# Performance work log

Hardware: AMD Instinct MI355X
Metric: run time of the kernel (lower is better)

## Reference

```python
import jax, jax.numpy as jnp
import numpy as np

L, D, V, F4 = 12, 768, 50304, 3072
B, T = 4, 1024


def setup_inputs() -> dict:
    key = jax.random.key(0)
    ks = jax.random.split(key, 12)
    s = 0.02
    return {
        "idx": jax.random.randint(ks[0], (B, T), 0, V),
        "targets": jax.random.randint(ks[1], (B, T), 0, V),
        "wte": jax.random.normal(ks[2], (V, D), jnp.float32) * s,  # tied with lm_head
        "pos_embed": jax.random.normal(ks[3], (L, D), jnp.float32),  # per-block (1,1,D) learned pos embed
        "dyt_alpha": jnp.full((L, 3), 0.5, jnp.float32),  # dyt, dyt2, dyt3 alphas
        "dyt_w": jnp.ones((L, 3, D), jnp.float32),
        "dyt_b": jnp.zeros((L, 3, D), jnp.float32),
        "Wq": jax.random.normal(ks[4], (L, D, D), jnp.float32) * s,
        "Wk": jax.random.normal(ks[5], (L, D, D), jnp.float32) * s,
        "Wv": jax.random.normal(ks[6], (L, D, D), jnp.float32) * s,
        "Wp": jax.random.normal(ks[7], (L, D, D), jnp.float32) * s,
        "bp": jnp.zeros((L, D), jnp.float32),
        "We": jax.random.normal(ks[8], (L, F4, D), jnp.float32) * s,
        "be": jnp.zeros((L, F4), jnp.float32),
        "Wc": jax.random.normal(ks[9], (L, D, F4), jnp.float32) * s,
        "bc": jnp.zeros((L, D), jnp.float32),
    }


def _dyt(x, a, w, b):
    return jnp.tanh(a * x) * w + b


def _forward(idx, targets, wte, pos_embed, dyt_alpha, dyt_w, dyt_b,
             Wq, Wk, Wv, Wp, bp, We, be, Wc, bc):
    b, t = idx.shape
    x = wte[idx]  # (b,t,D)
    pos = jnp.arange(t)
    pbias = -jnp.abs(pos[None, :] - pos[:, None]).astype(x.dtype)  # (t,t) ALiBi-style bias
    scale = 1.0 / np.sqrt(D)  # note: source scales by sqrt(emb_dim), not head dim
    total_kl = jnp.asarray(0.0, x.dtype)
    for l in range(L):
        xl = x + pos_embed[l][None, None, :]
        prior = _dyt(xl, dyt_alpha[l, 2], dyt_w[l, 2], dyt_b[l, 2])  # dyt3
        h = _dyt(xl, dyt_alpha[l, 0], dyt_w[l, 0], dyt_b[l, 0])      # dyt (dropout=0)
        Q = jnp.einsum('btd,od->bto', h, Wq[l])
        K = jnp.einsum('btd,od->bto', h, Wk[l])
        Vv = jnp.einsum('btd,od->bto', h, Wv[l])
        scores = jnp.einsum('btd,bsd->bts', Q, K) * scale + pbias  # (b,t,t), no causal mask
        aw = jax.nn.softmax(scores, axis=-1)
        ao = jnp.einsum('bts,bsd->btd', aw, Vv)
        ao = jnp.einsum('btd,od->bto', ao, Wp[l]) + bp[l]
        h2 = _dyt(ao, dyt_alpha[l, 1], dyt_w[l, 1], dyt_b[l, 1])     # dyt2
        h2 = jax.nn.gelu(jnp.einsum('btd,fd->btf', h2, We[l]) + be[l], approximate=False)
        h2 = jnp.einsum('btf,df->btd', h2, Wc[l]) + bc[l]
        posterior = h2 + prior
        m = 0.5 * (prior + posterior)
        lm = jax.nn.log_softmax(m, axis=-1)
        mp = jnp.exp(lm)
        lp = jax.nn.log_softmax(prior, axis=-1)
        lq = jax.nn.log_softmax(posterior, axis=-1)
        # F.kl_div(log_p, q, reduction='batchmean') = sum(q*(log q - log_p)) / batch
        kl = 0.5 * (jnp.sum(mp * (lm - lp)) + jnp.sum(mp * (lm - lq))) / b
        total_kl = total_kl + kl
        x = posterior
    logits = jnp.einsum('btd,vd->btv', x[:, -1:, :], wte)  # (b,1,V)
    full_logits = jnp.einsum('btd,vd->btv', x, wte)
    lsm = jax.nn.log_softmax(full_logits, axis=-1)
    nll = -jnp.take_along_axis(lsm, targets[..., None], axis=-1).squeeze(-1)
    loss = jnp.mean(nll) + total_kl * 0.1
    return logits, loss


def reference(idx, targets, wte, pos_embed, dyt_alpha, dyt_w, dyt_b,
              Wq, Wk, Wv, Wp, bp, We, be, Wc, bc):
    return _forward(idx, targets, wte, pos_embed, dyt_alpha, dyt_w, dyt_b,
                    Wq, Wk, Wv, Wp, bp, We, be, Wc, bc)
```

## Files before the change

### kernel.cpp

```cpp
#include <hip/hip_runtime.h>
#include <hip/hip_bf16.h>

typedef __attribute__((ext_vector_type(8))) short bf16x8;
typedef __attribute__((ext_vector_type(4))) float f32x4;

__device__ __forceinline__ short f2bf(float f) {
  unsigned u = __float_as_uint(f);
  u = u + 0x7fffu + ((u >> 16) & 1u);
  return (short)(u >> 16);
}
__device__ __forceinline__ float bf2f(short s) {
  return __uint_as_float(((unsigned)(unsigned short)s) << 16);
}

#define GLOB_CAST(p) ((const __attribute__((address_space(1))) void*)(p))
#define LDS_CAST(p) ((__attribute__((address_space(3))) void*)(p))
#define GLL16(g, l) __builtin_amdgcn_global_load_lds(GLOB_CAST(g), LDS_CAST(l), 16, 0, 0)

constexpr int EP_BF16 = 0, EP_SCORES = 1, EP_DYT = 2, EP_GELU = 3, EP_PRIOR = 4;

__global__ __launch_bounds__(256) void cvt_k(const float* __restrict__ src,
                                             short* __restrict__ dst, long n4) {
  const long s = (long)blockIdx.x * 256 + threadIdx.x;
  if (s >= n4) return;
  float4 v = ((const float4*)src)[s];
  short4 o = {f2bf(v.x), f2bf(v.y), f2bf(v.z), f2bf(v.w)};
  ((short4*)dst)[s] = o;
}

__global__ __launch_bounds__(256) void cvt_layer_k(
    const float* __restrict__ wq, const float* __restrict__ wk,
    const float* __restrict__ wv, const float* __restrict__ wp,
    const float* __restrict__ we, const float* __restrict__ wc,
    short* __restrict__ dst) {
  const long s = (long)blockIdx.x * 256 + threadIdx.x;
  const long e = s * 4;
  const float* src; long off;
  if (e < 589824)        { src = wq; off = e; }
  else if (e < 1179648)  { src = wk; off = e - 589824; }
  else if (e < 1769472)  { src = wv; off = e - 1179648; }
  else if (e < 2359296)  { src = wp; off = e - 1769472; }
  else if (e < 4718592)  { src = we; off = e - 2359296; }
  else                   { src = wc; off = e - 4718592; }
  float4 v = *(const float4*)(src + off);
  short4 o = {f2bf(v.x), f2bf(v.y), f2bf(v.z), f2bf(v.w)};
  *(short4*)(dst + e) = o;
}

__global__ __launch_bounds__(256) void embed_head_k(
    const int* __restrict__ idx, const float* __restrict__ wte,
    const float* __restrict__ pos, const float* __restrict__ alp,
    const float* __restrict__ w, const float* __restrict__ b,
    float* __restrict__ x, float* __restrict__ prior, short* __restrict__ h) {
  const long s = (long)blockIdx.x * 256 + threadIdx.x;
  const long row = s / 192;
  const int c4 = (int)(s % 192);
  float4 xv = ((const float4*)(wte + (long)idx[row] * 768))[c4];
  ((float4*)x)[s] = xv;
  float4 pv = ((const float4*)pos)[c4];
  float4 w0 = ((const float4*)w)[c4];
  float4 b0 = ((const float4*)b)[c4];
  float4 w2 = ((const float4*)(w + 1536))[c4];
  float4 b2 = ((const float4*)(b + 1536))[c4];
  const float a0 = alp[0], a2 = alp[2];
  float4 xl = {xv.x + pv.x, xv.y + pv.y, xv.z + pv.z, xv.w + pv.w};
  float4 pr = {tanhf(a2 * xl.x) * w2.x + b2.x, tanhf(a2 * xl.y) * w2.y + b2.y,
               tanhf(a2 * xl.z) * w2.z + b2.z, tanhf(a2 * xl.w) * w2.w + b2.w};
  ((float4*)prior)[s] = pr;
  short4 hh = {f2bf(tanhf(a0 * xl.x) * w0.x + b0.x),
               f2bf(tanhf(a0 * xl.y) * w0.y + b0.y),
               f2bf(tanhf(a0 * xl.z) * w0.z + b0.z),
               f2bf(tanhf(a0 * xl.w) * w0.w + b0.w)};
  ((short4*)h)[s] = hh;
}

template <int EP, int TN>
__global__ __launch_bounds__(256, 2) void gemm_bt(
    const short* __restrict__ A, const short* __restrict__ B,
    void* __restrict__ Cv, int K, int lda, int ldb, int ldc,
    long sA, long sB, long sC,
    const float* __restrict__ bias, const float* __restrict__ dw,
    const float* __restrict__ db, const float* __restrict__ alp,
    const float* __restrict__ prior, float scale) {
  constexpr int NF = TN / 32;
  __shared__ short As[128 * 64];
  __shared__ short Bs[TN * 64];
  const int tid = threadIdx.x, lane = tid & 63;
  const int wr = tid >> 7, wc = (tid >> 6) & 1;
  const long rowBase = (long)blockIdx.y * 128;
  const long colBase = (long)blockIdx.x * TN;
  const short* Ab = A + (long)blockIdx.z * sA;
  const short* Bb = B + (long)blockIdx.z * sB;
  const int srow = tid >> 3, sseg = tid & 7;
  const int ssegS = sseg ^ (srow & 7);

  f32x4 acc[4][NF];
#pragma unroll
  for (int m = 0; m < 4; ++m)
#pragma unroll
    for (int n = 0; n < NF; ++n) acc[m][n] = (f32x4){0.f, 0.f, 0.f, 0.f};

  const int q = lane >> 4, cl = lane & 15;
  const int rsw = cl & 7;

  for (int kt = 0; kt < K; kt += 64) {
#pragma unroll
    for (int i = 0; i < 4; ++i)
      GLL16(Ab + (rowBase + i * 32 + srow) * (long)lda + kt + ssegS * 8,
            As + ((i * 32 + srow) * 64 + sseg * 8));
#pragma unroll
    for (int i = 0; i < TN / 32; ++i)
      GLL16(Bb + (colBase + i * 32 + srow) * (long)ldb + kt + ssegS * 8,
            Bs + ((i * 32 + srow) * 64 + sseg * 8));
    __syncthreads();
#pragma unroll
    for (int kk = 0; kk < 2; ++kk) {
      const int sw = ((kk * 4 + q) ^ rsw) << 3;
      bf16x8 af[4], bfr[NF];
#pragma unroll
      for (int m = 0; m < 4; ++m)
        af[m] = *(const bf16x8*)&As[(wr * 64 + m * 16 + cl) * 64 + sw];
#pragma unroll
      for (int n = 0; n < NF; ++n)
        bfr[n] = *(const bf16x8*)&Bs[(wc * (TN / 2) + n * 16 + cl) * 64 + sw];
#pragma unroll
      for (int m = 0; m < 4; ++m)
#pragma unroll
        for (int n = 0; n < NF; ++n)
          acc[m][n] = __builtin_amdgcn_mfma_f32_16x16x32_bf16(af[m], bfr[n], acc[m][n], 0, 0, 0);
    }
    __syncthreads();
  }

#pragma unroll
  for (int m = 0; m < 4; ++m) {
#pragma unroll
    for (int n = 0; n < NF; ++n) {
#pragma unroll
      for (int j = 0; j < 4; ++j) {
        long r = rowBase + wr * 64 + m * 16 + q * 4 + j;
        long c = colBase + wc * (TN / 2) + n * 16 + cl;
        float v = acc[m][n][j];
        if constexpr (EP == EP_SCORES) {
          float pb = -fabsf((float)(int)(r - c));
          ((float*)Cv)[(long)blockIdx.z * sC + r * ldc + c] = v * scale + pb;
        } else if constexpr (EP == EP_BF16) {
          ((short*)Cv)[(long)blockIdx.z * sC + r * ldc + c] = f2bf(v);
        } else if constexpr (EP == EP_DYT) {
          float xv = v + bias[c];
          ((short*)Cv)[r * (long)ldc + c] = f2bf(tanhf(alp[0] * xv) * dw[c] + db[c]);
        } else if constexpr (EP == EP_GELU) {
          float xv = v + bias[c];
          ((short*)Cv)[r * (long)ldc + c] = f2bf(0.5f * xv * (1.f + erff(xv * 0.70710678118654752f)));
        } else if constexpr (EP == EP_PRIOR) {
          ((float*)Cv)[r * (long)ldc + c] = v + bias[c] + prior[r * (long)ldc + c];
        }
      }
    }
  }
}

__global__ __launch_bounds__(256) void transp_k(const short* __restrict__ V,
                                                short* __restrict__ Vt, int ldv) {
  __shared__ short t[32][33];
  const int b = blockIdx.z;
  const int d0 = blockIdx.x * 32, t0 = blockIdx.y * 32;
  const int tx = threadIdx.x & 31, ty = threadIdx.x >> 5;
  const short* Vb = V + (long)b * 1024 * ldv;
  short* Tb = Vt + (long)b * 768 * 1024;
#pragma unroll
  for (int i = 0; i < 4; ++i)
    t[ty + i * 8][tx] = Vb[(long)(t0 + ty + i * 8) * ldv + d0 + tx];
  __syncthreads();
#pragma unroll
  for (int i = 0; i < 4; ++i)
    Tb[(long)(d0 + ty + i * 8) * 1024 + t0 + tx] = t[tx][ty + i * 8];
}

__global__ __launch_bounds__(256) void softmax_k(float* __restrict__ sc) {
  const int lane = threadIdx.x & 63;
  const long row = (long)blockIdx.x * 4 + (threadIdx.x >> 6);
  const float4* p = (const float4*)(sc + row * 1024);
  float4 v[4];
  float mx = -3e38f;
#pragma unroll
  for (int i = 0; i < 4; ++i) {
    v[i] = p[lane * 4 + i];
    mx = fmaxf(mx, fmaxf(fmaxf(v[i].x, v[i].y), fmaxf(v[i].z, v[i].w)));
  }
#pragma unroll
  for (int o = 1; o < 64; o <<= 1) mx = fmaxf(mx, __shfl_xor(mx, o));
  float e[16];
  float s = 0.f;
#pragma unroll
  for (int i = 0; i < 4; ++i) {
    e[i * 4 + 0] = __expf(v[i].x - mx);
    e[i * 4 + 1] = __expf(v[i].y - mx);
    e[i * 4 + 2] = __expf(v[i].z - mx);
    e[i * 4 + 3] = __expf(v[i].w - mx);
    s += e[i * 4] + e[i * 4 + 1] + e[i * 4 + 2] + e[i * 4 + 3];
  }
#pragma unroll
  for (int o = 1; o < 64; o <<= 1) s += __shfl_xor(s, o);
  const float inv = 1.f / s;
  short4* dst = (short4*)((short*)sc + row * 2048);
#pragma unroll
  for (int i = 0; i < 4; ++i) {
    short4 o4 = {f2bf(e[i * 4] * inv), f2bf(e[i * 4 + 1] * inv),
                 f2bf(e[i * 4 + 2] * inv), f2bf(e[i * 4 + 3] * inv)};
    dst[lane * 4 + i] = o4;
  }
}

__global__ __launch_bounds__(256) void tail_k(
    float* __restrict__ prior, const float* __restrict__ post,
    const float* __restrict__ pos_n, const float* __restrict__ alp_n,
    const float* __restrict__ w_n, const float* __restrict__ b_n,
    short* __restrict__ h, short* __restrict__ xbf,
    double* __restrict__ acc, int last) {
  const int lane = threadIdx.x & 63;
  const long row = (long)blockIdx.x * 4 + (threadIdx.x >> 6);
  float* pp = prior + row * 768;
  const float* qq = post + row * 768;
  float p[12], q[12];
#pragma unroll
  for (int i = 0; i < 12; ++i) { p[i] = pp[lane + i * 64]; q[i] = qq[lane + i * 64]; }
  float mp = -3e38f, mq = -3e38f, mm = -3e38f;
#pragma unroll
  for (int i = 0; i < 12; ++i) {
    float m = 0.5f * (p[i] + q[i]);
    mp = fmaxf(mp, p[i]); mq = fmaxf(mq, q[i]); mm = fmaxf(mm, m);
  }
#pragma unroll
  for (int o = 1; o < 64; o <<= 1) {
    mp = fmaxf(mp, __shfl_xor(mp, o));
    mq = fmaxf(mq, __shfl_xor(mq, o));
    mm = fmaxf(mm, __shfl_xor(mm, o));
  }
  float sp = 0.f, sq = 0.f, sm = 0.f;
#pragma unroll
  for (int i = 0; i < 12; ++i) {
    sp += __expf(p[i] - mp);
    sq += __expf(q[i] - mq);
    sm += __expf(0.5f * (p[i] + q[i]) - mm);
  }
#pragma unroll
  for (int o = 1; o < 64; o <<= 1) {
    sp += __shfl_xor(sp, o); sq += __shfl_xor(sq, o); sm += __shfl_xor(sm, o);
  }
  const float lseP = mp + logf(sp), lseQ = mq + logf(sq), lseM = mm + logf(sm);
  float kl = 0.f;
#pragma unroll
  for (int i = 0; i < 12; ++i) {
    float m = 0.5f * (p[i] + q[i]);
    float lm = m - lseM;
    kl += __expf(lm) * (2.f * lm - (p[i] - lseP) - (q[i] - lseQ));
  }
#pragma unroll
  for (int o = 1; o < 64; o <<= 1) kl += __shfl_xor(kl, o);
  if (lane == 0) atomicAdd(&acc[0], (double)kl);

  if (last) {
#pragma unroll
    for (int i = 0; i < 12; ++i) xbf[row * 768 + lane + i * 64] = f2bf(q[i]);
  } else {
    const float a0 = alp_n[0], a2 = alp_n[2];
#pragma unroll
    for (int i = 0; i < 12; ++i) {
      const int col = lane + i * 64;
      float xl = q[i] + pos_n[col];
      pp[col] = tanhf(a2 * xl) * w_n[1536 + col] + b_n[1536 + col];
      h[row * 768 + col] = f2bf(tanhf(a0 * xl) * w_n[col] + b_n[col]);
    }
  }
}

__global__ __launch_bounds__(256, 2) void lse_gemm_k(
    const short* __restrict__ Xb, const short* __restrict__ Wt,
    float* __restrict__ pm, float* __restrict__ ps,
    float* __restrict__ logits_out, int G) {
  __shared__ short As[128 * 64];
  __shared__ short Bs[128 * 64];
  __shared__ float pmx[2][128], psm[2][128], rm[128], rs[128];
  const int tid = threadIdx.x, lane = tid & 63;
  const int wr = tid >> 7, wc = (tid >> 6) & 1;
  const int g = blockIdx.x;
  const long rowBase = (long)blockIdx.y * 128;
  const int srow = tid >> 3, sseg = tid & 7;
  const int ssegS = sseg ^ (srow & 7);
  const int q = lane >> 4, cl = lane & 15;
  const int rsw = cl & 7;
  if (tid < 128) { rm[tid] = -3e38f; rs[tid] = 0.f; }

  for (int tile = g; tile < 393; tile += G) {
    const long colBase = (long)tile * 128;
    f32x4 acc[4][4];
#pragma unroll
    for (int m = 0; m < 4; ++m)
#pragma unroll
      for (int n = 0; n < 4; ++n) acc[m][n] = (f32x4){0.f, 0.f, 0.f, 0.f};

    for (int kt = 0; kt < 768; kt += 64) {
#pragma unroll
      for (int i = 0; i < 4; ++i) {
        GLL16(Xb + (rowBase + i * 32 + srow) * 768L + kt + ssegS * 8,
              As + ((i * 32 + srow) * 64 + sseg * 8));
        GLL16(Wt + (colBase + i * 32 + srow) * 768L + kt + ssegS * 8,
              Bs + ((i * 32 + srow) * 64 + sseg * 8));
      }
      __syncthreads();
#pragma unroll
      for (int kk = 0; kk < 2; ++kk) {
        const int sw = ((kk * 4 + q) ^ rsw) << 3;
        bf16x8 af[4], bfr[4];
#pragma unroll
        for (int m = 0; m < 4; ++m)
          af[m] = *(const bf16x8*)&As[(wr * 64 + m * 16 + cl) * 64 + sw];
#pragma unroll
        for (int n = 0; n < 4; ++n)
          bfr[n] = *(const bf16x8*)&Bs[(wc * 64 + n * 16 + cl) * 64 + sw];
#pragma unroll
        for (int m = 0; m < 4; ++m)
#pragma unroll
          for (int n = 0; n < 4; ++n)
            acc[m][n] = __builtin_amdgcn_mfma_f32_16x16x32_bf16(af[m], bfr[n], acc[m][n], 0, 0, 0);
      }
      __syncthreads();
    }

#pragma unroll
    for (int m = 0; m < 4; ++m)
#pragma unroll
      for (int n = 0; n < 4; ++n)
#pragma unroll
        for (int j = 0; j < 4; ++j) {
          long r = rowBase + wr * 64 + m * 16 + q * 4 + j;
          if ((r & 1023) == 1023) {
            long c = colBase + wc * 64 + n * 16 + cl;
            logits_out[(r >> 10) * 50304 + c] = acc[m][n][j];
          }
        }

#pragma unroll
    for (int m = 0; m < 4; ++m) {
#pragma unroll
      for (int j = 0; j < 4; ++j) {
        float mx = acc[m][0][j];
#pragma unroll
        for (int n = 1; n < 4; ++n) mx = fmaxf(mx, acc[m][n][j]);
#pragma unroll
        for (int o = 1; o < 16; o <<= 1) mx = fmaxf(mx, __shfl_xor(mx, o));
        float sm = 0.f;
#pragma unroll
        for (int n = 0; n < 4; ++n) sm += __expf(acc[m][n][j] - mx);
#pragma unroll
        for (int o = 1; o < 16; o <<= 1) sm += __shfl_xor(sm, o);
        if (cl == 0) {
          int lr = wr * 64 + m * 16 + q * 4 + j;
          pmx[wc][lr] = mx;
          psm[wc][lr] = sm;
        }
      }
    }
    __syncthreads();
    if (tid < 128) {
      float m0 = pmx[0][tid], m1 = pmx[1][tid];
      float m2 = fmaxf(m0, m1);
      float s2 = psm[0][tid] * __expf(m0 - m2) + psm[1][tid] * __expf(m1 - m2);
      float mo = rm[tid], mn = fmaxf(mo, m2);
      rs[tid] = rs[tid] * __expf(mo - mn) + s2 * __expf(m2 - mn);
      rm[tid] = mn;
    }
    __syncthreads();
  }
  if (tid < 128) {
    long row = rowBase + tid;
    pm[row * G + g] = rm[tid];
    ps[row * G + g] = rs[tid];
  }
}

__global__ __launch_bounds__(256) void tlog_k(const short* __restrict__ xbf,
                                              const short* __restrict__ wtebf,
                                              const int* __restrict__ targets,
                                              float* __restrict__ tlog) {
  const int lane = threadIdx.x & 63;
  const long row = (long)blockIdx.x * 4 + (threadIdx.x >> 6);
  const long tgt = targets[row];
  const short* a = xbf + row * 768;
  const short* b = wtebf + tgt * 768;
  float s = 0.f;
#pragma unroll
  for (int i = 0; i < 12; ++i) s += bf2f(a[lane + i * 64]) * bf2f(b[lane + i * 64]);
#pragma unroll
  for (int o = 1; o < 64; o <<= 1) s += __shfl_xor(s, o);
  if (lane == 0) tlog[row] = s;
}

__global__ __launch_bounds__(256) void stage2_k(const float* __restrict__ pm,
                                                const float* __restrict__ ps,
                                                const float* __restrict__ tlog,
                                                double* __restrict__ acc, int G) {
  const long row = (long)blockIdx.x * 256 + threadIdx.x;
  float M = -3e38f;
  for (int gi = 0; gi < G; ++gi) M = fmaxf(M, pm[row * G + gi]);
  float S = 0.f;
  for (int gi = 0; gi < G; ++gi) S += ps[row * G + gi] * __expf(pm[row * G + gi] - M);
  float nll = (M + logf(S)) - tlog[row];
#pragma unroll
  for (int o = 1; o < 64; o <<= 1) nll += __shfl_xor(nll, o);
  if ((threadIdx.x & 63) == 0) atomicAdd(&acc[1], (double)nll);
}

__global__ void finalize_k(const double* __restrict__ acc, float* __restrict__ out) {
  if (threadIdx.x == 0)
    out[201216] = (float)(acc[1] / 4096.0 + 0.1 * 0.5 * acc[0] / 4.0);
}

constexpr size_t OFF_WTEBF = 0;
constexpr size_t OFF_LW    = 77266944;
constexpr size_t OFF_X     = 91422720;
constexpr size_t OFF_PRIOR = 104005632;
constexpr size_t OFF_HB    = 116588544;
constexpr size_t OFF_U1    = 122880000;
constexpr size_t OFF_QKV   = OFF_U1;
constexpr size_t OFF_VT    = OFF_U1 + 18874368;
constexpr size_t OFF_E     = OFF_U1;
constexpr size_t OFF_SC    = 148045824;
constexpr size_t OFF_AO    = 164823040;
constexpr size_t OFF_XBF   = 171114496;
constexpr size_t OFF_PM    = 177405952;
constexpr size_t OFF_PS    = 177799168;
constexpr size_t OFF_TLOG  = 178192384;
constexpr size_t OFF_ACC   = 178208768;
constexpr size_t WS_NEED   = 178208784;

extern "C" void kernel_launch(void* const* d_in, const int* in_sizes, int n_in,
                              void* d_out, int out_size, void* d_ws, size_t ws_size,
                              hipStream_t stream) {
  const int* idx = (const int*)d_in[0];
  const int* targets = (const int*)d_in[1];
  const float* wte = (const float*)d_in[2];
  const float* pos = (const float*)d_in[3];
  const float* dalpha = (const float*)d_in[4];
  const float* dytw = (const float*)d_in[5];
  const float* dytb = (const float*)d_in[6];
  const float* Wq = (const float*)d_in[7];
  const float* Wk = (const float*)d_in[8];
  const float* Wv = (const float*)d_in[9];
  const float* Wp = (const float*)d_in[10];
  const float* bp = (const float*)d_in[11];
  const float* We = (const float*)d_in[12];
  const float* be = (const float*)d_in[13];
  const float* Wc = (const float*)d_in[14];
  const float* bc = (const float*)d_in[15];
  float* out = (float*)d_out;

  if (ws_size < WS_NEED) return;
  char* ws = (char*)d_ws;
  short* WTEBF = (short*)(ws + OFF_WTEBF);
  short* LW = (short*)(ws + OFF_LW);
  float* X = (float*)(ws + OFF_X);
  float* PRIOR = (float*)(ws + OFF_PRIOR);
  short* HB = (short*)(ws + OFF_HB);
  short* QKVB = (short*)(ws + OFF_QKV);
  short* VT = (short*)(ws + OFF_VT);
  short* E = (short*)(ws + OFF_E);
  float* SC = (float*)(ws + OFF_SC);
  short* AW = (short*)(ws + OFF_SC);
  short* AO = (short*)(ws + OFF_AO);
  short* XBF = (short*)(ws + OFF_XBF);
  float* PM = (float*)(ws + OFF_PM);
  float* PS = (float*)(ws + OFF_PS);
  float* TLOG = (float*)(ws + OFF_TLOG);
  double* ACC = (double*)(ws + OFF_ACC);

  hipMemsetAsync(ACC, 0, 16, stream);
  cvt_k<<<37728, 256, 0, stream>>>(wte, WTEBF, 9658368);
  embed_head_k<<<3072, 256, 0, stream>>>(idx, wte, pos, dalpha, dytw, dytb, X, PRIOR, HB);

  const float scale = 0.03608439182435161f;

  for (int l = 0; l < 12; ++l) {
    cvt_layer_k<<<6912, 256, 0, stream>>>(Wq + (long)l * 589824, Wk + (long)l * 589824,
                                          Wv + (long)l * 589824, Wp + (long)l * 589824,
                                          We + (long)l * 2359296, Wc + (long)l * 2359296, LW);
    gemm_bt<EP_BF16, 128><<<dim3(18, 32, 1), 256, 0, stream>>>(
        HB, LW, QKVB, 768, 768, 768, 2304, 0, 0, 0,
        nullptr, nullptr, nullptr, nullptr, nullptr, 0.f);
    transp_k<<<dim3(24, 32, 4), 256, 0, stream>>>(QKVB + 1536, VT, 2304);
    gemm_bt<EP_SCORES, 64><<<dim3(16, 8, 4), 256, 0, stream>>>(
        QKVB, QKVB + 768, SC, 768, 2304, 2304, 1024,
        2359296, 2359296, 1048576, nullptr, nullptr, nullptr, nullptr, nullptr, scale);
    softmax_k<<<1024, 256, 0, stream>>>(SC);
    gemm_bt<EP_BF16, 64><<<dim3(12, 8, 4), 256, 0, stream>>>(
        AW, VT, AO, 1024, 2048, 1024, 768, 2097152, 786432, 786432,
        nullptr, nullptr, nullptr, nullptr, nullptr, 0.f);
    gemm_bt<EP_DYT, 64><<<dim3(12, 32, 1), 256, 0, stream>>>(
        AO, LW + 1769472, HB, 768, 768, 768, 768, 0, 0, 0,
        bp + l * 768, dytw + l * 2304 + 768, dytb + l * 2304 + 768,
        dalpha + l * 3 + 1, nullptr, 0.f);
    gemm_bt<EP_GELU, 128><<<dim3(24, 32, 1), 256, 0, stream>>>(
        HB, LW + 2359296, E, 768, 768, 768, 3072, 0, 0, 0,
        be + l * 3072, nullptr, nullptr, nullptr, nullptr, 0.f);
    gemm_bt<EP_PRIOR, 64><<<dim3(12, 32, 1), 256, 0, stream>>>(
        E, LW + 4718592, X, 3072, 3072, 3072, 768, 0, 0, 0,
        bc + l * 768, nullptr, nullptr, nullptr, PRIOR, 0.f);
    tail_k<<<1024, 256, 0, stream>>>(PRIOR, X, pos + (l + 1) * 768,
                                     dalpha + (l + 1) * 3, dytw + (l + 1) * 2304,
                                     dytb + (l + 1) * 2304, HB, XBF, ACC, l == 11);
  }

  lse_gemm_k<<<dim3(24, 32), 256, 0, stream>>>(XBF, WTEBF, PM, PS, out, 24);
  tlog_k<<<1024, 256, 0, stream>>>(XBF, WTEBF, targets, TLOG);
  stage2_k<<<16, 256, 0, stream>>>(PM, PS, TLOG, ACC, 24);
  finalize_k<<<1, 64, 0, stream>>>(ACC, out);
}
```

Measured before the change: 3.111 ms.

## Rewrite LM-head logsumexp GEMM with 256x256 tiles and double-buffered LDS pipeline

Replaces the final vocab-projection logsumexp GEMM with a 512-thread kernel using 256x256 output tiles, double-buffered LDS staging spread across four sub-steps with explicit vmcnt waits, and raised scheduling priority around the MFMA blocks. The vocab dimension is padded to a multiple of 256 by zeroing extra rows of the bf16 embedding table, and padded columns are masked out of the max/sum. The goal is more data reuse per loaded byte and overlap of global loads with matrix math in the largest GEMM. In exchange it uses more LDS and registers per block, launches fewer blocks (256), and the workspace offsets shift to make room for the padding.

```diff
diff --git a/kernel.cpp b/kernel.cpp
--- a/kernel.cpp
+++ b/kernel.cpp
@@ -275,105 +275,156 @@
   }
 }
 
-__global__ __launch_bounds__(256, 2) void lse_gemm_k(
+__global__ __launch_bounds__(512, 1) void lse8_k(
     const short* __restrict__ Xb, const short* __restrict__ Wt,
     float* __restrict__ pm, float* __restrict__ ps,
     float* __restrict__ logits_out, int G) {
-  __shared__ short As[128 * 64];
-  __shared__ short Bs[128 * 64];
-  __shared__ float pmx[2][128], psm[2][128], rm[128], rs[128];
-  const int tid = threadIdx.x, lane = tid & 63;
-  const int wr = tid >> 7, wc = (tid >> 6) & 1;
+  __shared__ short As[2][256 * 64];
+  __shared__ short Bs[2][256 * 64];
+  __shared__ float pmx[4][256], psm[4][256], rm[256], rs[256];
+  const int tid = threadIdx.x;
+  const int lane = tid & 63, wid = tid >> 6;
+  const int wr = wid >> 2, wc = wid & 3;
+  const int q4 = lane >> 4, cl = lane & 15;
+  const long rowBase = (long)blockIdx.y * 256;
   const int g = blockIdx.x;
-  const long rowBase = (long)blockIdx.y * 128;
   const int srow = tid >> 3, sseg = tid & 7;
   const int ssegS = sseg ^ (srow & 7);
-  const int q = lane >> 4, cl = lane & 15;
-  const int rsw = cl & 7;
-  if (tid < 128) { rm[tid] = -3e38f; rs[tid] = 0.f; }
-
-  for (int tile = g; tile < 393; tile += G) {
-    const long colBase = (long)tile * 128;
-    f32x4 acc[4][4];
-#pragma unroll
-    for (int m = 0; m < 4; ++m)
+
+  if (tid < 256) { rm[tid] = -3e38f; rs[tid] = 0.f; }
+  __syncthreads();
+
+#define STAGE_A(slot, kt, half)                                              \
+  {                                                                          \
+    _Pragma("unroll") for (int i_ = 0; i_ < 2; ++i_) {                       \
+      int row_ = i_ * 128 + (half) * 64 + srow;                              \
+      GLL16(Xb + (rowBase + row_) * 768L + (kt) + ssegS * 8,                 \
+            &As[slot][row_ * 64 + sseg * 8]);                                \
+    }                                                                        \
+  }
+#define STAGE_B(slot, kt, half)                                              \
+  {                                                                          \
+    _Pragma("unroll") for (int i_ = 0; i_ < 2; ++i_) {                       \
+      int row_ = i_ * 128 + (srow >> 5) * 64 + (half) * 32 + (srow & 31);    \
+      GLL16(Wt + (colBase + row_) * 768L + (kt) + ssegS * 8,                 \
+            &Bs[slot][row_ * 64 + sseg * 8]);                                \
+    }                                                                        \
+  }
+
+#pragma unroll 1
+  for (int tile = g; tile < 197; tile += G) {
+    const long colBase = (long)tile * 256;
+    f32x4 acc[8][4];
+#pragma unroll
+    for (int m = 0; m < 8; ++m)
 #pragma unroll
       for (int n = 0; n < 4; ++n) acc[m][n] = (f32x4){0.f, 0.f, 0.f, 0.f};
 
-    for (int kt = 0; kt < 768; kt += 64) {
-#pragma unroll
-      for (int i = 0; i < 4; ++i) {
-        GLL16(Xb + (rowBase + i * 32 + srow) * 768L + kt + ssegS * 8,
-              As + ((i * 32 + srow) * 64 + sseg * 8));
-        GLL16(Wt + (colBase + i * 32 + srow) * 768L + kt + ssegS * 8,
-              Bs + ((i * 32 + srow) * 64 + sseg * 8));
+    STAGE_A(0, 0, 0); STAGE_B(0, 0, 0); STAGE_B(0, 0, 1); STAGE_A(0, 0, 1);
+
+#pragma unroll 1
+    for (int u = 0; u < 12; ++u) {
+      const int cur = u & 1, nxt = cur ^ 1;
+      const int ktn = (u + 1) * 64;
+      const bool stg = (u + 1) < 12;
+#pragma unroll
+      for (int q = 0; q < 4; ++q) {
+        if (q == 0) {
+          asm volatile("s_waitcnt vmcnt(4)" ::: "memory");
+        } else if (q == 1) {
+          if (stg) asm volatile("s_waitcnt vmcnt(2)" ::: "memory");
+          else     asm volatile("s_waitcnt vmcnt(0)" ::: "memory");
+        } else if (q == 2 && !stg) {
+          asm volatile("s_waitcnt vmcnt(0)" ::: "memory");
+        }
+        __builtin_amdgcn_s_barrier();
+        asm volatile("" ::: "memory");
+        if (stg) {
+          if (q == 0)      STAGE_A(nxt, ktn, 0)
+          else if (q == 1) STAGE_B(nxt, ktn, 0)
+          else if (q == 2) STAGE_B(nxt, ktn, 1)
+          else             STAGE_A(nxt, ktn, 1)
+        }
+        const int a = q >> 1, b = q & 1;
+        bf16x8 af[4][2], bfr[2][2];
+#pragma unroll
+        for (int mf = 0; mf < 4; ++mf)
+#pragma unroll
+          for (int kk = 0; kk < 2; ++kk) {
+            int row = wr * 128 + (a * 4 + mf) * 16 + cl;
+            int s = ((kk * 4 + q4) ^ (cl & 7)) << 3;
+            af[mf][kk] = *(const bf16x8*)&As[cur][row * 64 + s];
+          }
+#pragma unroll
+        for (int nf = 0; nf < 2; ++nf)
+#pragma unroll
+          for (int kk = 0; kk < 2; ++kk) {
+            int row = wc * 64 + (b * 2 + nf) * 16 + cl;
+            int s = ((kk * 4 + q4) ^ (cl & 7)) << 3;
+            bfr[nf][kk] = *(const bf16x8*)&Bs[cur][row * 64 + s];
+          }
+        __builtin_amdgcn_s_setprio(1);
+#pragma unroll
+        for (int mf = 0; mf < 4; ++mf)
+#pragma unroll
+          for (int nf = 0; nf < 2; ++nf)
+#pragma unroll
+            for (int kk = 0; kk < 2; ++kk)
+              acc[a * 4 + mf][b * 2 + nf] = __builtin_amdgcn_mfma_f32_16x16x32_bf16(
+                  af[mf][kk], bfr[nf][kk], acc[a * 4 + mf][b * 2 + nf], 0, 0, 0);
+        __builtin_amdgcn_s_setprio(0);
       }
-      __syncthreads();
-#pragma unroll
-      for (int kk = 0; kk < 2; ++kk) {
-        const int sw = ((kk * 4 + q) ^ rsw) << 3;
-        bf16x8 af[4], bfr[4];
-#pragma unroll
-        for (int m = 0; m < 4; ++m)
-          af[m] = *(const bf16x8*)&As[(wr * 64 + m * 16 + cl) * 64 + sw];
-#pragma unroll
-        for (int n = 0; n < 4; ++n)
-          bfr[n] = *(const bf16x8*)&Bs[(wc * 64 + n * 16 + cl) * 64 + sw];
-#pragma unroll
-        for (int m = 0; m < 4; ++m)
-#pragma unroll
-          for (int n = 0; n < 4; ++n)
-            acc[m][n] = __builtin_amdgcn_mfma_f32_16x16x32_bf16(af[m], bfr[n], acc[m][n], 0, 0, 0);
-      }
-      __syncthreads();
     }
 
 #pragma unroll
-    for (int m = 0; m < 4; ++m)
-#pragma unroll
-      for (int n = 0; n < 4; ++n)
-#pragma unroll
-        for (int j = 0; j < 4; ++j) {
-          long r = rowBase + wr * 64 + m * 16 + q * 4 + j;
-          if ((r & 1023) == 1023) {
-            long c = colBase + wc * 64 + n * 16 + cl;
-            logits_out[(r >> 10) * 50304 + c] = acc[m][n][j];
-          }
+    for (int mf = 0; mf < 8; ++mf) {
+#pragma unroll
+      for (int j = 0; j < 4; ++j) {
+        long r = rowBase + wr * 128 + mf * 16 + q4 * 4 + j;
+        float vv[4];
+        float mx = -3e38f;
+#pragma unroll
+        for (int nf = 0; nf < 4; ++nf) {
+          long c = colBase + wc * 64 + nf * 16 + cl;
+          float v = acc[mf][nf][j];
+          if ((r & 1023) == 1023 && c < 50304)
+            logits_out[(r >> 10) * 50304 + c] = v;
+          vv[nf] = (c < 50304) ? v : -3e38f;
+          mx = fmaxf(mx, vv[nf]);
         }
-
-#pragma unroll
-    for (int m = 0; m < 4; ++m) {
-#pragma unroll
-      for (int j = 0; j < 4; ++j) {
-        float mx = acc[m][0][j];
-#pragma unroll
-        for (int n = 1; n < 4; ++n) mx = fmaxf(mx, acc[m][n][j]);
 #pragma unroll
         for (int o = 1; o < 16; o <<= 1) mx = fmaxf(mx, __shfl_xor(mx, o));
         float sm = 0.f;
 #pragma unroll
-        for (int n = 0; n < 4; ++n) sm += __expf(acc[m][n][j] - mx);
+        for (int nf = 0; nf < 4; ++nf)
+          sm += (vv[nf] > -1e38f) ? __expf(vv[nf] - mx) : 0.f;
 #pragma unroll
         for (int o = 1; o < 16; o <<= 1) sm += __shfl_xor(sm, o);
         if (cl == 0) {
-          int lr = wr * 64 + m * 16 + q * 4 + j;
+          int lr = wr * 128 + mf * 16 + q4 * 4 + j;
           pmx[wc][lr] = mx;
           psm[wc][lr] = sm;
         }
       }
     }
     __syncthreads();
-    if (tid < 128) {
-      float m0 = pmx[0][tid], m1 = pmx[1][tid];
-      float m2 = fmaxf(m0, m1);
-      float s2 = psm[0][tid] * __expf(m0 - m2) + psm[1][tid] * __expf(m1 - m2);
+    if (tid < 256) {
+      float m2 = fmaxf(fmaxf(pmx[0][tid], pmx[1][tid]), fmaxf(pmx[2][tid], pmx[3][tid]));
+      float s2 = 0.f;
+#pragma unroll
+      for (int w = 0; w < 4; ++w)
+        s2 += (pmx[w][tid] > -1e38f) ? psm[w][tid] * __expf(pmx[w][tid] - m2) : 0.f;
       float mo = rm[tid], mn = fmaxf(mo, m2);
-      rs[tid] = rs[tid] * __expf(mo - mn) + s2 * __expf(m2 - mn);
-      rm[tid] = mn;
+      if (mn > -1e38f) {
+        rs[tid] = rs[tid] * __expf(mo - mn) + s2 * __expf(m2 - mn);
+        rm[tid] = mn;
+      }
     }
     __syncthreads();
   }
-  if (tid < 128) {
+#undef STAGE_A
+#undef STAGE_B
+  if (tid < 256) {
     long row = rowBase + tid;
     pm[row * G + g] = rm[tid];
     ps[row * G + g] = rs[tid];
@@ -418,22 +469,22 @@
 }
 
 constexpr size_t OFF_WTEBF = 0;
-constexpr size_t OFF_LW    = 77266944;
-constexpr size_t OFF_X     = 91422720;
-constexpr size_t OFF_PRIOR = 104005632;
-constexpr size_t OFF_HB    = 116588544;
-constexpr size_t OFF_U1    = 122880000;
+constexpr size_t OFF_LW    = 77463552;
+constexpr size_t OFF_X     = 91619328;
+constexpr size_t OFF_PRIOR = 104202240;
+constexpr size_t OFF_HB    = 116785152;
+constexpr size_t OFF_U1    = 123076608;
 constexpr size_t OFF_QKV   = OFF_U1;
 constexpr size_t OFF_VT    = OFF_U1 + 18874368;
 constexpr size_t OFF_E     = OFF_U1;
-constexpr size_t OFF_SC    = 148045824;
-constexpr size_t OFF_AO    = 164823040;
-constexpr size_t OFF_XBF   = 171114496;
-constexpr size_t OFF_PM    = 177405952;
-constexpr size_t OFF_PS    = 177799168;
-constexpr size_t OFF_TLOG  = 178192384;
-constexpr size_t OFF_ACC   = 178208768;
-constexpr size_t WS_NEED   = 178208784;
+constexpr size_t OFF_SC    = 148242432;
+constexpr size_t OFF_AO    = 165019648;
+constexpr size_t OFF_XBF   = 171311104;
+constexpr size_t OFF_PM    = 177602560;
+constexpr size_t OFF_PS    = 177864704;
+constexpr size_t OFF_TLOG  = 178126848;
+constexpr size_t OFF_ACC   = 178143232;
+constexpr size_t WS_NEED   = 178143248;
 
 extern "C" void kernel_launch(void* const* d_in, const int* in_sizes, int n_in,
                               void* d_out, int out_size, void* d_ws, size_t ws_size,
@@ -476,6 +527,7 @@
   double* ACC = (double*)(ws + OFF_ACC);
 
   hipMemsetAsync(ACC, 0, 16, stream);
+  hipMemsetAsync(WTEBF + 50304L * 768, 0, 128L * 768 * 2, stream);
   cvt_k<<<37728, 256, 0, stream>>>(wte, WTEBF, 9658368);
   embed_head_k<<<3072, 256, 0, stream>>>(idx, wte, pos, dalpha, dytw, dytb, X, PRIOR, HB);
 
@@ -511,8 +563,8 @@
                                      dytb + (l + 1) * 2304, HB, XBF, ACC, l == 11);
   }
 
-  lse_gemm_k<<<dim3(24, 32), 256, 0, stream>>>(XBF, WTEBF, PM, PS, out, 24);
+  lse8_k<<<dim3(16, 16), 512, 0, stream>>>(XBF, WTEBF, PM, PS, out, 16);
   tlog_k<<<1024, 256, 0, stream>>>(XBF, WTEBF, targets, TLOG);
-  stage2_k<<<16, 256, 0, stream>>>(PM, PS, TLOG, ACC, 24);
+  stage2_k<<<16, 256, 0, stream>>>(PM, PS, TLOG, ACC, 16);
   finalize_k<<<1, 64, 0, stream>>>(ACC, out);
 }
```

Measured after the change: 3.396 ms. +9.2%, slower.
